# Optimization experiments

Hardware: AMD Instinct MI355X
Metric: run time of the kernel (lower is better)

Reference implementation:

```python
import jax, jax.numpy as jnp
import numpy as np

NH = 16  # num_attention_heads
DH = 64  # attention_head_size
HS = 1024
LN_EPS = 1e-5


def _linear(x, W, b):
    return jnp.einsum('bsh,oh->bso', x, W) + b


def _mha(q, k, v, mask):
    # q:[B,Sq,H] k,v:[B,Sk,H] mask:[B,Sk] int (1=keep,0=mask)
    B, Sq, _ = q.shape
    Sk = k.shape[1]
    qh = q.reshape(B, Sq, NH, DH).transpose(0, 2, 1, 3)
    kh = k.reshape(B, Sk, NH, DH).transpose(0, 2, 1, 3)
    vh = v.reshape(B, Sk, NH, DH).transpose(0, 2, 1, 3)
    scores = jnp.einsum('bhqd,bhkd->bhqk', qh, kh) / np.sqrt(DH).astype(np.float32)
    if mask is not None:
        scores = jnp.where(mask[:, None, None, :] == 0, jnp.float32(-1e9), scores)
    probs = jax.nn.softmax(scores, axis=-1)  # dropout is identity in eval
    ctx = jnp.einsum('bhqk,bhkd->bhqd', probs, vh)
    return ctx.transpose(0, 2, 1, 3).reshape(B, Sq, NH * DH)


def _layernorm(x, g, b):
    mu = jnp.mean(x, axis=-1, keepdims=True)
    var = jnp.mean(jnp.square(x - mu), axis=-1, keepdims=True)
    return (x - mu) * jax.lax.rsqrt(var + LN_EPS) * g + b


def setup_inputs() -> dict:
    key = jax.random.key(0)
    ks = jax.random.split(key, 20)
    B, Sc, Se = 4, 512, 2048
    s = 0.02
    inp = {
        'claim_embeddings': jax.random.normal(ks[0], (B, Sc, HS), jnp.float32),
        'evidence_embeddings': jax.random.normal(ks[1], (B, Se, HS), jnp.float32),
        'claim_mask': jax.random.randint(ks[2], (B, Sc), 0, 2, jnp.int32),
        'evidence_mask': jax.random.randint(ks[3], (B, Se), 0, 2, jnp.int32),
    }
    names = ['cq', 'ek', 'ev', 'eq', 'ck', 'cv']
    for i, n in enumerate(names):
        inp['W_' + n] = jax.random.normal(ks[4 + i], (HS, HS), jnp.float32) * s
        inp['b_' + n] = jnp.zeros((HS,), jnp.float32)
    inp['ln_g'] = jnp.ones((HS,), jnp.float32)
    inp['ln_b'] = jnp.zeros((HS,), jnp.float32)
    return inp


def reference(claim_embeddings, evidence_embeddings, claim_mask, evidence_mask,
              W_cq, b_cq, W_ek, b_ek, W_ev, b_ev,
              W_eq, b_eq, W_ck, b_ck, W_cv, b_cv, ln_g, ln_b):
    claim_att = _mha(_linear(claim_embeddings, W_cq, b_cq),
                     _linear(evidence_embeddings, W_ek, b_ek),
                     _linear(evidence_embeddings, W_ev, b_ev), evidence_mask)
    evid_att = _mha(_linear(evidence_embeddings, W_eq, b_eq),
                    _linear(claim_embeddings, W_ck, b_ck),
                    _linear(claim_embeddings, W_cv, b_cv), claim_mask)
    claim_out = _layernorm(claim_embeddings + claim_att, ln_g, ln_b)
    evid_out = _layernorm(evidence_embeddings + evid_att, ln_g, ln_b)
    return (claim_out, evid_out)
```

## Files before the change

kernel.cpp:

```cpp
#include <hip/hip_runtime.h>
#include <hip/hip_bf16.h>
#include <stdint.h>

typedef __hip_bfloat16 bf16;
typedef __attribute__((ext_vector_type(8))) short bf16x8;
typedef __attribute__((ext_vector_type(4))) float f32x4;

#define DEV __device__ __forceinline__

DEV float lo_bf(unsigned int v) { union { unsigned int u; float f; } c; c.u = v << 16; return c.f; }
DEV float hi_bf(unsigned int v) { union { unsigned int u; float f; } c; c.u = v & 0xffff0000u; return c.f; }
DEV float bs2f(short h) { union { unsigned int u; float f; } c; c.u = ((unsigned int)(unsigned short)h) << 16; return c.f; }

DEV int probe_bf16(const void* ln_g) { return ((const uint16_t*)ln_g)[0] == 0x3F80; }

DEV unsigned short f2bs(float f) { union { bf16 h; unsigned short s; } u; u.h = __float2bfloat16(f); return u.s; }

DEV float ldf(const void* p, size_t i, int bfm) {
    return bfm ? __bfloat162float(((const bf16*)p)[i]) : ((const float*)p)[i];
}

DEV bf16x8 pack8(float4 x, float4 y) {
    union { unsigned short s[8]; bf16x8 v; } u;
    u.s[0] = f2bs(x.x); u.s[1] = f2bs(x.y); u.s[2] = f2bs(x.z); u.s[3] = f2bs(x.w);
    u.s[4] = f2bs(y.x); u.s[5] = f2bs(y.y); u.s[6] = f2bs(y.z); u.s[7] = f2bs(y.w);
    return u.v;
}

DEV bf16x8 ld8cvt(const void* p, size_t i, int bfm) {
    if (bfm) return *(const bf16x8*)((const bf16*)p + i);
    const float4* f = (const float4*)((const float*)p + i);
    return pack8(f[0], f[1]);
}

DEV void gload_lds16(const bf16* g, bf16* l) {
    __builtin_amdgcn_global_load_lds(
        (const __attribute__((address_space(1))) void*)g,
        (__attribute__((address_space(3))) void*)l,
        16, 0, 0);
}

template<int CTRL>
DEV float dpp_ror(float x) {
    union { float f; int i; } u; u.f = x;
    const int r = __builtin_amdgcn_update_dpp(0, u.i, CTRL, 0xf, 0xf, false);
    union { int i; float f; } w; w.i = r; return w.f;
}

__global__ __launch_bounds__(256) void conv_bf16(
    const void* __restrict__ Xc, const void* __restrict__ Xe,
    const void* __restrict__ W0, const void* __restrict__ W1, const void* __restrict__ W2,
    const void* __restrict__ W3, const void* __restrict__ W4, const void* __restrict__ W5,
    bf16* __restrict__ dst, const void* __restrict__ probe)
{
    const int bfm = probe_bf16(probe);
    const size_t tot = (size_t)16384 * 1024;
    const size_t step = (size_t)gridDim.x * 256 * 8;
    for (size_t e = ((size_t)blockIdx.x * 256 + threadIdx.x) * 8; e < tot; e += step) {
        const size_t row = e >> 10;
        const void* src; size_t off;
        if (row < 2048)       { src = Xc; off = e; }
        else if (row < 10240) { src = Xe; off = e - (size_t)2048 * 1024; }
        else {
            const int wi = (int)((row - 10240) >> 10);
            src = (wi == 0) ? W0 : (wi == 1) ? W1 : (wi == 2) ? W2 :
                  (wi == 3) ? W3 : (wi == 4) ? W4 : W5;
            off = e - (size_t)(10240 + wi * 1024) * 1024;
        }
        *(bf16x8*)(dst + e) = ld8cvt(src, off, bfm);
    }
}

__global__ __launch_bounds__(256) void gemm_fast(
    const bf16* __restrict__ AW,
    const void* __restrict__ B0, const void* __restrict__ B1, const void* __restrict__ B2,
    const void* __restrict__ B3, const void* __restrict__ B4, const void* __restrict__ B5,
    bf16* __restrict__ Out, const void* __restrict__ probe)
{
    __shared__ __align__(16) bf16 As[2][128 * 32];
    __shared__ __align__(16) bf16 Bs[2][128 * 32];

    const int bfm = probe_bf16(probe);
    const int L = (blockIdx.x & 7) * 240 + (blockIdx.x >> 3);
    const int z  = L / 640;
    const int rem = L % 640;
    const int bx = rem >> 3;
    const int by = rem & 7;
    const int rowBase = bx * 128;
    const int colBase = by * 128;
    const int ev = rowBase >= 2048;
    const int widx = z * 2 + ev;

    const bf16* Ap = AW;
    const bf16* Wp = AW + (size_t)(10240 + widx * 1024) * 1024;
    const void* bias = (widx == 0) ? B0 : (widx == 1) ? B1 : (widx == 2) ? B2 :
                       (widx == 3) ? B3 : (widx == 4) ? B4 : B5;
    bf16* O = Out + (size_t)z * 10240 * 1024;

    const int tid  = threadIdx.x;
    const int wave = tid >> 6;
    const int lane = tid & 63;
    const int wm   = wave >> 1;
    const int wn   = wave & 1;
    const int quad = lane >> 4;
    const int l16  = lane & 15;

    f32x4 acc[4][4];
#pragma unroll
    for (int i = 0; i < 4; i++)
#pragma unroll
        for (int j = 0; j < 4; j++) acc[i][j] = (f32x4){0.f, 0.f, 0.f, 0.f};

    const int sr = tid >> 2;
    const int sc = (tid & 3) * 8;
    const size_t ga = (size_t)(rowBase + sr) * 1024 + sc;
    const size_t gb = (size_t)(colBase + sr) * 1024 + sc;

    auto stage = [&](int buf, int k0) {
        gload_lds16(Ap + ga + k0,                     &As[buf][tid * 8]);
        gload_lds16(Ap + ga + (size_t)64 * 1024 + k0, &As[buf][2048 + tid * 8]);
        gload_lds16(Wp + gb + k0,                     &Bs[buf][tid * 8]);
        gload_lds16(Wp + gb + (size_t)64 * 1024 + k0, &Bs[buf][2048 + tid * 8]);
    };

    stage(0, 0);
    __syncthreads();

    int cur = 0;
    for (int k0 = 0; k0 < 1024; k0 += 32) {
        if (k0 + 32 < 1024) stage(cur ^ 1, k0 + 32);

        bf16x8 af[4], bfr[4];
#pragma unroll
        for (int i = 0; i < 4; i++) {
            af[i]  = *(const bf16x8*)(&As[cur][(wm * 64 + i * 16 + l16) * 32 + quad * 8]);
            bfr[i] = *(const bf16x8*)(&Bs[cur][(wn * 64 + i * 16 + l16) * 32 + quad * 8]);
        }
#pragma unroll
        for (int i = 0; i < 4; i++)
#pragma unroll
            for (int j = 0; j < 4; j++)
                acc[i][j] = __builtin_amdgcn_mfma_f32_16x16x32_bf16(af[i], bfr[j], acc[i][j], 0, 0, 0);

        __syncthreads();
        cur ^= 1;
    }

#pragma unroll
    for (int j = 0; j < 4; j++) {
        const int col = colBase + wn * 64 + j * 16 + l16;
        const float bv = ldf(bias, col, bfm);
#pragma unroll
        for (int i = 0; i < 4; i++) {
            const int row0 = rowBase + wm * 64 + i * 16 + quad * 4;
#pragma unroll
            for (int rr = 0; rr < 4; rr++)
                O[(size_t)(row0 + rr) * 1024 + col] = __float2bfloat16(acc[i][j][rr] + bv);
        }
    }
}

DEV void attn_core(const bf16* __restrict__ Q, const bf16* __restrict__ K,
                   const bf16* __restrict__ V, const int* __restrict__ mask,
                   bf16* __restrict__ O, int Sk, int h, int qRow0)
{
    __shared__ __align__(16) short Ks [64 * 72];
    __shared__ __align__(16) short VTs[64 * 72];
    __shared__ __align__(16) short Ps [4][16 * 72];

    const int tid  = threadIdx.x;
    const int w    = tid >> 6;
    const int lane = tid & 63;
    const int quad = lane >> 4;
    const int l16  = lane & 15;
    const int qRow = qRow0 + w * 16 + l16;

    const short* Qp = (const short*)Q + (size_t)qRow * 1024 + h * 64;
    const bf16x8 qf0 = *(const bf16x8*)(Qp + quad * 8);
    const bf16x8 qf1 = *(const bf16x8*)(Qp + 32 + quad * 8);

    bf16x8 ones8;
#pragma unroll
    for (int i = 0; i < 8; i++) ones8[i] = (short)0x3F80;

    f32x4 oacc[4];
#pragma unroll
    for (int dt = 0; dt < 4; dt++) oacc[dt] = (f32x4){0.f, 0.f, 0.f, 0.f};
    f32x4 lacc = (f32x4){0.f, 0.f, 0.f, 0.f};
    float mrun[4] = {-3e38f, -3e38f, -3e38f, -3e38f};

    const int sn = tid >> 2, sseg = tid & 3;
    const int vn2 = (tid & 31) * 2;
    const int vdg = tid >> 5;

    bf16x8 pk0, pk1, pv0, pv1;
    auto loadkv = [&](int k0) {
        const short* src = (const short*)K + (size_t)(k0 + sn) * 1024 + h * 64 + sseg * 16;
        pk0 = *(const bf16x8*)src;
        pk1 = *(const bf16x8*)(src + 8);
        const short* vsrc = (const short*)V + (size_t)(k0 + vn2) * 1024 + h * 64 + vdg * 8;
        pv0 = *(const bf16x8*)vsrc;
        pv1 = *(const bf16x8*)(vsrc + 1024);
    };
    loadkv(0);

    const float SCL = 0.18033688f;

    for (int k0 = 0; k0 < Sk; k0 += 64) {
        __syncthreads();
        *(bf16x8*)(Ks + sn * 72 + sseg * 16)     = pk0;
        *(bf16x8*)(Ks + sn * 72 + sseg * 16 + 8) = pk1;
#pragma unroll
        for (int i = 0; i < 8; i++) {
            const unsigned int pr = (unsigned short)pv0[i] |
                                    ((unsigned int)(unsigned short)pv1[i] << 16);
            *(unsigned int*)(VTs + (vdg * 8 + i) * 72 + vn2) = pr;
        }
        __syncthreads();
        {
            int kn = k0 + 64; if (kn >= Sk) kn = 0;
            loadkv(kn);
        }

        const int mv_all = mask[k0 + lane];

        f32x4 sacc[4];
#pragma unroll
        for (int t = 0; t < 4; t++) {
            const bf16x8 kf0 = *(const bf16x8*)(Ks + (t * 16 + l16) * 72 + quad * 8);
            const bf16x8 kf1 = *(const bf16x8*)(Ks + (t * 16 + l16) * 72 + 32 + quad * 8);
            f32x4 s = (f32x4){0.f, 0.f, 0.f, 0.f};
            s = __builtin_amdgcn_mfma_f32_16x16x32_bf16(qf0, kf0, s, 0, 0, 0);
            s = __builtin_amdgcn_mfma_f32_16x16x32_bf16(qf1, kf1, s, 0, 0, 0);
            const int mv = __shfl(mv_all, t * 16 + l16);
#pragma unroll
            for (int r = 0; r < 4; r++) sacc[t][r] = mv ? s[r] * SCL : -1e9f;
        }

        float cmax[4];
#pragma unroll
        for (int r = 0; r < 4; r++) {
            cmax[r] = fmaxf(fmaxf(sacc[0][r], sacc[1][r]), fmaxf(sacc[2][r], sacc[3][r]));
            cmax[r] = fmaxf(cmax[r], dpp_ror<0x121>(cmax[r]));
            cmax[r] = fmaxf(cmax[r], dpp_ror<0x122>(cmax[r]));
            cmax[r] = fmaxf(cmax[r], dpp_ror<0x124>(cmax[r]));
            cmax[r] = fmaxf(cmax[r], dpp_ror<0x128>(cmax[r]));
        }

        float alpha[4];
#pragma unroll
        for (int r = 0; r < 4; r++) {
            const float mn = fmaxf(mrun[r], cmax[r]);
            alpha[r] = exp2f(mrun[r] - mn);
            mrun[r] = mn;
        }
#pragma unroll
        for (int t = 0; t < 4; t++)
#pragma unroll
            for (int r = 0; r < 4; r++) {
                const float p = exp2f(sacc[t][r] - mrun[r]);
                Ps[w][(quad * 4 + r) * 72 + t * 16 + l16] = f2bs(p);
            }
#pragma unroll
        for (int r = 0; r < 4; r++) lacc[r] *= alpha[r];
#pragma unroll
        for (int dt = 0; dt < 4; dt++)
#pragma unroll
            for (int r = 0; r < 4; r++) oacc[dt][r] *= alpha[r];


        const bf16x8 pa0 = *(const bf16x8*)(Ps[w] + l16 * 72 + quad * 8);
        const bf16x8 pa1 = *(const bf16x8*)(Ps[w] + l16 * 72 + 32 + quad * 8);
        lacc = __builtin_amdgcn_mfma_f32_16x16x32_bf16(pa0, ones8, lacc, 0, 0, 0);
        lacc = __builtin_amdgcn_mfma_f32_16x16x32_bf16(pa1, ones8, lacc, 0, 0, 0);
#pragma unroll
        for (int dt = 0; dt < 4; dt++) {
            const bf16x8 vb0 = *(const bf16x8*)(VTs + (dt * 16 + l16) * 72 + quad * 8);
            const bf16x8 vb1 = *(const bf16x8*)(VTs + (dt * 16 + l16) * 72 + 32 + quad * 8);
            oacc[dt] = __builtin_amdgcn_mfma_f32_16x16x32_bf16(pa0, vb0, oacc[dt], 0, 0, 0);
            oacc[dt] = __builtin_amdgcn_mfma_f32_16x16x32_bf16(pa1, vb1, oacc[dt], 0, 0, 0);
        }
    }

    short* Op = (short*)O;
#pragma unroll
    for (int r = 0; r < 4; r++) {
        const float inv = 1.0f / lacc[r];
        const size_t row = (size_t)(qRow0 + w * 16 + quad * 4 + r) * 1024 + h * 64;
#pragma unroll
        for (int dt = 0; dt < 4; dt++)
            Op[row + dt * 16 + l16] = f2bs(oacc[dt][r] * inv);
    }
}

__global__ __launch_bounds__(256) void attn_flat(
    const bf16* __restrict__ Q1, const bf16* __restrict__ K1, const bf16* __restrict__ V1,
    const int* __restrict__ m1, bf16* __restrict__ O1,
    const bf16* __restrict__ Q2, const bf16* __restrict__ K2, const bf16* __restrict__ V2,
    const int* __restrict__ m2, bf16* __restrict__ O2)
{
    const int xcd = blockIdx.x & 7;
    const int idx = blockIdx.x >> 3;
    const int grp = idx / 5;
    const int pos = idx % 5;

    if (pos == 0) {
        const int j = xcd * 64 + grp;
        const int b = j >> 7;
        const int h = (j >> 3) & 15;
        const int qRow0 = (j & 7) * 64;
        attn_core(Q1 + (size_t)b * 512 * 1024,
                  K1 + (size_t)b * 2048 * 1024,
                  V1 + (size_t)b * 2048 * 1024,
                  m1 + (size_t)b * 2048,
                  O1 + (size_t)b * 512 * 1024, 2048, h, qRow0);
    } else {
        const int j = xcd * 256 + grp * 4 + (pos - 1);
        const int b = j >> 9;
        const int h = (j >> 5) & 15;
        const int qRow0 = (j & 31) * 64;
        attn_core(Q2 + (size_t)b * 2048 * 1024,
                  K2 + (size_t)b * 512 * 1024,
                  V2 + (size_t)b * 512 * 1024,
                  m2 + (size_t)b * 512,
                  O2 + (size_t)b * 2048 * 1024, 512, h, qRow0);
    }
}

__global__ __launch_bounds__(256) void attn_dual(
    const bf16* __restrict__ Q1, const bf16* __restrict__ K1, const bf16* __restrict__ V1,
    const int* __restrict__ m1, bf16* __restrict__ O1,
    const bf16* __restrict__ Q2, const bf16* __restrict__ K2, const bf16* __restrict__ V2,
    const int* __restrict__ m2, bf16* __restrict__ O2)
{
    const int z = blockIdx.z;
    if (z < 4) {
        if (blockIdx.x >= 8) return;
        attn_core(Q1 + (size_t)z * 512 * 1024,
                  K1 + (size_t)z * 2048 * 1024,
                  V1 + (size_t)z * 2048 * 1024,
                  m1 + (size_t)z * 2048,
                  O1 + (size_t)z * 512 * 1024, 2048, blockIdx.y, blockIdx.x * 64);
    } else {
        const int b = z - 4;
        attn_core(Q2 + (size_t)b * 2048 * 1024,
                  K2 + (size_t)b * 512 * 1024,
                  V2 + (size_t)b * 512 * 1024,
                  m2 + (size_t)b * 512,
                  O2 + (size_t)b * 2048 * 1024, 512, blockIdx.y, blockIdx.x * 64);
    }
}

DEV void gemm_core(const void* __restrict__ A, int aRow0,
                   const void* __restrict__ W, const void* __restrict__ bias,
                   bf16* __restrict__ O, int bfm)
{
    __shared__ __align__(16) short As [128 * 40];
    __shared__ __align__(16) short Bsh[128 * 40];

    const int tid  = threadIdx.x;
    const int wave = tid >> 6;
    const int lane = tid & 63;
    const int wm   = wave >> 1;
    const int wn   = wave & 1;
    const int quad = lane >> 4;
    const int l16  = lane & 15;

    const int rowBase = blockIdx.x * 128;
    const int colBase = blockIdx.y * 128;

    f32x4 acc[4][4];
#pragma unroll
    for (int i = 0; i < 4; i++)
#pragma unroll
        for (int j = 0; j < 4; j++) acc[i][j] = (f32x4){0.f, 0.f, 0.f, 0.f};

    const int r  = tid >> 2;
    const int c8 = (tid & 3) * 8;
    const size_t aIdx = (size_t)(aRow0 + rowBase + r) * 1024 + c8;
    const size_t wIdx = (size_t)(colBase + r) * 1024 + c8;
    short* sA0 = As  + r * 40 + c8;
    short* sA1 = As  + (r + 64) * 40 + c8;
    short* sB0 = Bsh + r * 40 + c8;
    short* sB1 = Bsh + (r + 64) * 40 + c8;

    auto compute = [&]() {
        bf16x8 af[4], bfr[4];
#pragma unroll
        for (int i = 0; i < 4; i++) {
            af[i]  = *(const bf16x8*)(As  + (wm * 64 + i * 16 + l16) * 40 + quad * 8);
            bfr[i] = *(const bf16x8*)(Bsh + (wn * 64 + i * 16 + l16) * 40 + quad * 8);
        }
#pragma unroll
        for (int i = 0; i < 4; i++)
#pragma unroll
            for (int j = 0; j < 4; j++)
                acc[i][j] = __builtin_amdgcn_mfma_f32_16x16x32_bf16(af[i], bfr[j], acc[i][j], 0, 0, 0);
    };

    if (bfm) {
        const bf16* Ab = (const bf16*)A;
        const bf16* Wb = (const bf16*)W;
        bf16x8 ra0 = *(const bf16x8*)(Ab + aIdx);
        bf16x8 ra1 = *(const bf16x8*)(Ab + aIdx + (size_t)64 * 1024);
        bf16x8 rb0 = *(const bf16x8*)(Wb + wIdx);
        bf16x8 rb1 = *(const bf16x8*)(Wb + wIdx + (size_t)64 * 1024);
        for (int k0 = 0; k0 < 1024; k0 += 32) {
            __syncthreads();
            *(bf16x8*)sA0 = ra0; *(bf16x8*)sA1 = ra1;
            *(bf16x8*)sB0 = rb0; *(bf16x8*)sB1 = rb1;
            __syncthreads();
            const int kn = (k0 + 32) & 1023;
            ra0 = *(const bf16x8*)(Ab + aIdx + kn);
            ra1 = *(const bf16x8*)(Ab + aIdx + (size_t)64 * 1024 + kn);
            rb0 = *(const bf16x8*)(Wb + wIdx + kn);
            rb1 = *(const bf16x8*)(Wb + wIdx + (size_t)64 * 1024 + kn);
            compute();
        }
    } else {
        const float* Af = (const float*)A;
        const float* Wf = (const float*)W;
        float4 f[4][2];
        auto loadf = [&](int k) {
            f[0][0] = *(const float4*)(Af + aIdx + k);
            f[0][1] = *(const float4*)(Af + aIdx + k + 4);
            f[1][0] = *(const float4*)(Af + aIdx + (size_t)64 * 1024 + k);
            f[1][1] = *(const float4*)(Af + aIdx + (size_t)64 * 1024 + k + 4);
            f[2][0] = *(const float4*)(Wf + wIdx + k);
            f[2][1] = *(const float4*)(Wf + wIdx + k + 4);
            f[3][0] = *(const float4*)(Wf + wIdx + (size_t)64 * 1024 + k);
            f[3][1] = *(const float4*)(Wf + wIdx + (size_t)64 * 1024 + k + 4);
        };
        loadf(0);
        for (int k0 = 0; k0 < 1024; k0 += 32) {
            const bf16x8 ra0 = pack8(f[0][0], f[0][1]);
            const bf16x8 ra1 = pack8(f[1][0], f[1][1]);
            const bf16x8 rb0 = pack8(f[2][0], f[2][1]);
            const bf16x8 rb1 = pack8(f[3][0], f[3][1]);
            __syncthreads();
            *(bf16x8*)sA0 = ra0; *(bf16x8*)sA1 = ra1;
            *(bf16x8*)sB0 = rb0; *(bf16x8*)sB1 = rb1;
            __syncthreads();
            loadf((k0 + 32) & 1023);
            compute();
        }
    }

#pragma unroll
    for (int j = 0; j < 4; j++) {
        const int col = colBase + wn * 64 + j * 16 + l16;
        const float bv = ldf(bias, col, bfm);
#pragma unroll
        for (int i = 0; i < 4; i++) {
            const int row0 = rowBase + wm * 64 + i * 16 + quad * 4;
#pragma unroll
            for (int rr = 0; rr < 4; rr++)
                O[(size_t)(row0 + rr) * 1024 + col] = __float2bfloat16(acc[i][j][rr] + bv);
        }
    }
}

__global__ __launch_bounds__(256) void gemm_bt6(
    const void* __restrict__ Ac, const void* __restrict__ Ae,
    const void* __restrict__ W0, const void* __restrict__ W1, const void* __restrict__ W2,
    const void* __restrict__ W3, const void* __restrict__ W4, const void* __restrict__ W5,
    const void* __restrict__ B0, const void* __restrict__ B1, const void* __restrict__ B2,
    const void* __restrict__ B3, const void* __restrict__ B4, const void* __restrict__ B5,
    bf16* __restrict__ O0, bf16* __restrict__ O1, bf16* __restrict__ O2,
    bf16* __restrict__ O3, bf16* __restrict__ O4, bf16* __restrict__ O5,
    const void* __restrict__ dt_probe)
{
    const int z = blockIdx.z;
    if (z < 3 && blockIdx.x >= 16) return;
    const int bfm = probe_bf16(dt_probe);
    const void* A = (z < 3) ? Ac : Ae;
    const void* W    = (z == 0) ? W0 : (z == 1) ? W1 : (z == 2) ? W2 : (z == 3) ? W3 : (z == 4) ? W4 : W5;
    const void* bias = (z == 0) ? B0 : (z == 1) ? B1 : (z == 2) ? B2 : (z == 3) ? B3 : (z == 4) ? B4 : B5;
    bf16* O          = (z == 0) ? O0 : (z == 1) ? O1 : (z == 2) ? O2 : (z == 3) ? O3 : (z == 4) ? O4 : O5;
    gemm_core(A, 0, W, bias, O, bfm);
}

__global__ __launch_bounds__(256) void ln_wave(
    const void* __restrict__ Xc, const void* __restrict__ Xe, const bf16* __restrict__ Att,
    const void* __restrict__ G, const void* __restrict__ Bb, void* __restrict__ O)
{
    const int bfm = probe_bf16(G);
    const int lane = threadIdx.x & 63;
    const size_t row = (size_t)blockIdx.x * 4 + (threadIdx.x >> 6);
    const void* X; size_t xrow;
    if (row < 2048) { X = Xc; xrow = row; }
    else            { X = Xe; xrow = row - 2048; }

    const int e0 = lane * 16;
    float v[16];
    {
        const short* ap = (const short*)Att + row * 1024 + e0;
        const bf16x8 a0 = *(const bf16x8*)ap;
        const bf16x8 a1 = *(const bf16x8*)(ap + 8);
#pragma unroll
        for (int j = 0; j < 8; j++) { v[j] = bs2f(a0[j]); v[8 + j] = bs2f(a1[j]); }
    }
    if (bfm) {
        const short* xp = (const short*)X + xrow * 1024 + e0;
        const bf16x8 x0 = *(const bf16x8*)xp;
        const bf16x8 x1 = *(const bf16x8*)(xp + 8);
#pragma unroll
        for (int j = 0; j < 8; j++) { v[j] += bs2f(x0[j]); v[8 + j] += bs2f(x1[j]); }
    } else {
        const float* xp = (const float*)X + xrow * 1024 + e0;
#pragma unroll
        for (int q = 0; q < 4; q++) {
            const float4 f = *(const float4*)(xp + q * 4);
            v[q * 4 + 0] += f.x; v[q * 4 + 1] += f.y;
            v[q * 4 + 2] += f.z; v[q * 4 + 3] += f.w;
        }
    }

    float s = 0.f, ss = 0.f;
#pragma unroll
    for (int j = 0; j < 16; j++) { s += v[j]; ss += v[j] * v[j]; }
#pragma unroll
    for (int off = 32; off > 0; off >>= 1) {
        s  += __shfl_xor(s,  off);
        ss += __shfl_xor(ss, off);
    }
    const float mu   = s * (1.f / 1024.f);
    const float var  = ss * (1.f / 1024.f) - mu * mu;
    const float rstd = rsqrtf(var + 1e-5f);

    float g[16], bb[16];
    if (bfm) {
        const short* gp = (const short*)G + e0;
        const short* bp = (const short*)Bb + e0;
        const bf16x8 g0 = *(const bf16x8*)gp, g1 = *(const bf16x8*)(gp + 8);
        const bf16x8 b0 = *(const bf16x8*)bp, b1 = *(const bf16x8*)(bp + 8);
#pragma unroll
        for (int j = 0; j < 8; j++) {
            g[j] = bs2f(g0[j]); g[8 + j] = bs2f(g1[j]);
            bb[j] = bs2f(b0[j]); bb[8 + j] = bs2f(b1[j]);
        }
    } else {
        const float* gp = (const float*)G + e0;
        const float* bp = (const float*)Bb + e0;
#pragma unroll
        for (int q = 0; q < 4; q++) {
            const float4 gf = *(const float4*)(gp + q * 4);
            const float4 bf = *(const float4*)(bp + q * 4);
            g[q * 4 + 0] = gf.x; g[q * 4 + 1] = gf.y; g[q * 4 + 2] = gf.z; g[q * 4 + 3] = gf.w;
            bb[q * 4 + 0] = bf.x; bb[q * 4 + 1] = bf.y; bb[q * 4 + 2] = bf.z; bb[q * 4 + 3] = bf.w;
        }
    }

    float o[16];
#pragma unroll
    for (int j = 0; j < 16; j++) o[j] = (v[j] - mu) * rstd * g[j] + bb[j];

    const size_t obase = row * 1024 + e0;
    if (bfm) {
        union { unsigned short sh[16]; uint4 u[2]; } pk;
#pragma unroll
        for (int j = 0; j < 16; j++) pk.sh[j] = f2bs(o[j]);
        uint4* op = (uint4*)((bf16*)O + obase);
        op[0] = pk.u[0]; op[1] = pk.u[1];
    } else {
        float* op = (float*)O + obase;
#pragma unroll
        for (int q = 0; q < 4; q++)
            *(float4*)(op + q * 4) = (float4){o[q * 4], o[q * 4 + 1], o[q * 4 + 2], o[q * 4 + 3]};
    }
}

DEV void ln_body(const void* __restrict__ X, size_t xrow, const bf16* __restrict__ Att,
                 size_t arow, const void* __restrict__ G, const void* __restrict__ Bb,
                 void* __restrict__ O, size_t orow, int bfm)
{
    __shared__ float r1[4], r2[4];
    const int tid = threadIdx.x;
    const size_t abase = arow * 1024 + tid * 4;
    const size_t xbase = xrow * 1024 + tid * 4;
    const uint2 ab = *(const uint2*)(Att + abase);
    const float v0 = ldf(X, xbase + 0, bfm) + lo_bf(ab.x);
    const float v1 = ldf(X, xbase + 1, bfm) + hi_bf(ab.x);
    const float v2 = ldf(X, xbase + 2, bfm) + lo_bf(ab.y);
    const float v3 = ldf(X, xbase + 3, bfm) + hi_bf(ab.y);
    float s  = v0 + v1 + v2 + v3;
    float ss = v0 * v0 + v1 * v1 + v2 * v2 + v3 * v3;
    for (int off = 32; off > 0; off >>= 1) { s += __shfl_down(s, off); ss += __shfl_down(ss, off); }
    if ((tid & 63) == 0) { r1[tid >> 6] = s; r2[tid >> 6] = ss; }
    __syncthreads();
    const float S  = r1[0] + r1[1] + r1[2] + r1[3];
    const float SS = r2[0] + r2[1] + r2[2] + r2[3];
    const float mu   = S * (1.f / 1024.f);
    const float var  = SS * (1.f / 1024.f) - mu * mu;
    const float rstd = rsqrtf(var + 1e-5f);
    const float g0 = ldf(G, tid * 4 + 0, bfm), g1 = ldf(G, tid * 4 + 1, bfm);
    const float g2 = ldf(G, tid * 4 + 2, bfm), g3 = ldf(G, tid * 4 + 3, bfm);
    const float bb0 = ldf(Bb, tid * 4 + 0, bfm), bb1 = ldf(Bb, tid * 4 + 1, bfm);
    const float bb2 = ldf(Bb, tid * 4 + 2, bfm), bb3 = ldf(Bb, tid * 4 + 3, bfm);
    const float o0 = (v0 - mu) * rstd * g0 + bb0;
    const float o1 = (v1 - mu) * rstd * g1 + bb1;
    const float o2 = (v2 - mu) * rstd * g2 + bb2;
    const float o3 = (v3 - mu) * rstd * g3 + bb3;
    const size_t obase = orow * 1024 + tid * 4;
    if (bfm) {
        union { unsigned short s4[4]; uint2 u; } pack;
        pack.s4[0] = f2bs(o0); pack.s4[1] = f2bs(o1); pack.s4[2] = f2bs(o2); pack.s4[3] = f2bs(o3);
        *(uint2*)((bf16*)O + obase) = pack.u;
    } else {
        *(float4*)((float*)O + obase) = (float4){o0, o1, o2, o3};
    }
}

__global__ __launch_bounds__(256) void ln_kernel(
    const void* __restrict__ X, int xRow0, const bf16* __restrict__ Att,
    const void* __restrict__ G, const void* __restrict__ Bb,
    void* __restrict__ O, size_t oRow0)
{
    const int bfm = probe_bf16(G);
    const size_t row = blockIdx.x;
    ln_body(X, (size_t)xRow0 + row, Att, row, G, Bb, O, oRow0 + row, bfm);
}

extern "C" void kernel_launch(void* const* d_in, const int* in_sizes, int n_in,
                              void* d_out, int out_size, void* d_ws, size_t ws_size,
                              hipStream_t stream)
{
    (void)in_sizes; (void)n_in; (void)out_size;

    const void* c_emb  = d_in[0];
    const void* e_emb  = d_in[1];
    const int*  c_mask = (const int*)d_in[2];
    const int*  e_mask = (const int*)d_in[3];
    const void* W_cq = d_in[4];  const void* b_cq = d_in[5];
    const void* W_ek = d_in[6];  const void* b_ek = d_in[7];
    const void* W_ev = d_in[8];  const void* b_ev = d_in[9];
    const void* W_eq = d_in[10]; const void* b_eq = d_in[11];
    const void* W_ck = d_in[12]; const void* b_ck = d_in[13];
    const void* W_cv = d_in[14]; const void* b_cv = d_in[15];
    const void* ln_g = d_in[16]; const void* ln_b = d_in[17];

    const int B = 4, Scl = 512, Sev = 2048;
    const size_t MC = (size_t)B * Scl;
    const size_t ME = (size_t)B * Sev;
    const size_t MT = MC + ME;
    const size_t RW = MT * 1024;

    dim3 blk(256);
    const size_t need_fast = (3 * RW + (size_t)16384 * 1024) * sizeof(bf16);

    if (ws_size >= need_fast) {
        bf16* Qr = (bf16*)d_ws;
        bf16* Kr = Qr + RW;
        bf16* Vr = Kr + RW;
        bf16* CV = Vr + RW;

        conv_bf16<<<dim3(2048), blk, 0, stream>>>(
            c_emb, e_emb, W_cq, W_eq, W_ck, W_ek, W_cv, W_ev, CV, ln_g);

        gemm_fast<<<dim3(1920), blk, 0, stream>>>(
            CV, b_cq, b_eq, b_ck, b_ek, b_cv, b_ev, Qr, ln_g);

        attn_flat<<<dim3(2560), blk, 0, stream>>>(
            Qr,             Kr + MC * 1024, Vr + MC * 1024, e_mask, Qr,
            Qr + MC * 1024, Kr,             Vr,             c_mask, Qr + MC * 1024);

        ln_wave<<<dim3((unsigned)(MT / 4)), blk, 0, stream>>>(
            c_emb, e_emb, Qr, ln_g, ln_b, d_out);
    } else {
        bf16* q_c = (bf16*)d_ws;
        bf16* k_c = q_c + MC * 1024;
        bf16* v_c = k_c + MC * 1024;
        bf16* q_e = v_c + MC * 1024;
        bf16* k_e = q_e + ME * 1024;
        bf16* v_e = k_e + ME * 1024;

        gemm_bt6<<<dim3(64, 8, 6), blk, 0, stream>>>(
            c_emb, e_emb,
            W_cq, W_ck, W_cv, W_eq, W_ek, W_ev,
            b_cq, b_ck, b_cv, b_eq, b_ek, b_ev,
            q_c, k_c, v_c, q_e, k_e, v_e, ln_g);

        attn_dual<<<dim3(32, 16, 8), blk, 0, stream>>>(
            q_c, k_e, v_e, e_mask, q_c,
            q_e, k_c, v_c, c_mask, q_e);

        ln_kernel<<<dim3((unsigned)MC), blk, 0, stream>>>(
            c_emb, 0, q_c, ln_g, ln_b, d_out, 0);
        ln_kernel<<<dim3((unsigned)ME), blk, 0, stream>>>(
            e_emb, 0, q_e, ln_g, ln_b, d_out, MC);
    }
}
```

Baseline: 389.5 us.

## Stage GEMM and attention epilogues through LDS for coalesced stores; fold mask into MFMA init

The GEMM and attention epilogues now write their results into shared memory first and then emit 16-byte vectorized, coalesced global stores, instead of scattered 2-byte stores. The attention mask is applied as an additive bias in the MFMA accumulator initializer. The softmax scale is folded into an fmaf inside the native exp2 builtin, which removes a per-element select and multiply. These changes add extra __syncthreads and reuse of the staging LDS buffers. They also slightly change how masked scores interact with the scale (-1e9 is now scaled).

```diff
diff --git a/kernel.cpp b/kernel.cpp
--- a/kernel.cpp
+++ b/kernel.cpp
@@ -1,6 +1,7 @@
 #include <hip/hip_runtime.h>
 #include <hip/hip_bf16.h>
 #include <stdint.h>
+#include <math.h>
 
 typedef __hip_bfloat16 bf16;
 typedef __attribute__((ext_vector_type(8))) short bf16x8;
@@ -146,17 +147,30 @@
         cur ^= 1;
     }
 
+    bf16* Cme = (wn == 0) ? &As[0][0] : &Bs[0][0];
 #pragma unroll
     for (int j = 0; j < 4; j++) {
-        const int col = colBase + wn * 64 + j * 16 + l16;
-        const float bv = ldf(bias, col, bfm);
+        const int c64 = j * 16 + l16;
+        const float bv = ldf(bias, colBase + wn * 64 + c64, bfm);
 #pragma unroll
         for (int i = 0; i < 4; i++) {
-            const int row0 = rowBase + wm * 64 + i * 16 + quad * 4;
+            const int row0 = wm * 64 + i * 16 + quad * 4;
 #pragma unroll
             for (int rr = 0; rr < 4; rr++)
-                O[(size_t)(row0 + rr) * 1024 + col] = __float2bfloat16(acc[i][j][rr] + bv);
-        }
+                Cme[(row0 + rr) * 64 + c64] = __float2bfloat16(acc[i][j][rr] + bv);
+        }
+    }
+    __syncthreads();
+    const int srow = tid >> 3;
+    const int seg  = tid & 7;
+#pragma unroll
+    for (int pass = 0; pass < 4; pass++) {
+        const int row = pass * 32 + srow;
+        const bf16x8 v0 = *(const bf16x8*)(&As[0][0] + row * 64 + seg * 8);
+        const bf16x8 v1 = *(const bf16x8*)(&Bs[0][0] + row * 64 + seg * 8);
+        bf16* orow = O + (size_t)(rowBase + row) * 1024 + colBase;
+        *(bf16x8*)(orow + seg * 8)      = v0;
+        *(bf16x8*)(orow + 64 + seg * 8) = v1;
     }
 }
 
@@ -229,12 +243,11 @@
         for (int t = 0; t < 4; t++) {
             const bf16x8 kf0 = *(const bf16x8*)(Ks + (t * 16 + l16) * 72 + quad * 8);
             const bf16x8 kf1 = *(const bf16x8*)(Ks + (t * 16 + l16) * 72 + 32 + quad * 8);
-            f32x4 s = (f32x4){0.f, 0.f, 0.f, 0.f};
+            const float mb = __shfl(mv_all, t * 16 + l16) ? 0.f : -1e9f;
+            f32x4 s = (f32x4){mb, mb, mb, mb};
             s = __builtin_amdgcn_mfma_f32_16x16x32_bf16(qf0, kf0, s, 0, 0, 0);
             s = __builtin_amdgcn_mfma_f32_16x16x32_bf16(qf1, kf1, s, 0, 0, 0);
-            const int mv = __shfl(mv_all, t * 16 + l16);
-#pragma unroll
-            for (int r = 0; r < 4; r++) sacc[t][r] = mv ? s[r] * SCL : -1e9f;
+            sacc[t] = s;
         }
 
         float cmax[4];
@@ -247,18 +260,19 @@
             cmax[r] = fmaxf(cmax[r], dpp_ror<0x128>(cmax[r]));
         }
 
-        float alpha[4];
+        float alpha[4], mscl[4];
 #pragma unroll
         for (int r = 0; r < 4; r++) {
             const float mn = fmaxf(mrun[r], cmax[r]);
-            alpha[r] = exp2f(mrun[r] - mn);
+            alpha[r] = __builtin_amdgcn_exp2f((mrun[r] - mn) * SCL);
             mrun[r] = mn;
+            mscl[r] = mn * SCL;
         }
 #pragma unroll
         for (int t = 0; t < 4; t++)
 #pragma unroll
             for (int r = 0; r < 4; r++) {
-                const float p = exp2f(sacc[t][r] - mrun[r]);
+                const float p = __builtin_amdgcn_exp2f(fmaf(sacc[t][r], SCL, -mscl[r]));
                 Ps[w][(quad * 4 + r) * 72 + t * 16 + l16] = f2bs(p);
             }
 #pragma unroll
@@ -282,14 +296,24 @@
         }
     }
 
-    short* Op = (short*)O;
+    __syncthreads();
 #pragma unroll
     for (int r = 0; r < 4; r++) {
         const float inv = 1.0f / lacc[r];
-        const size_t row = (size_t)(qRow0 + w * 16 + quad * 4 + r) * 1024 + h * 64;
+        const int orow = w * 16 + quad * 4 + r;
 #pragma unroll
         for (int dt = 0; dt < 4; dt++)
-            Op[row + dt * 16 + l16] = f2bs(oacc[dt][r] * inv);
+            Ks[orow * 72 + dt * 16 + l16] = (short)f2bs(oacc[dt][r] * inv);
+    }
+    __syncthreads();
+    const int srow = tid >> 3;
+    const int seg  = tid & 7;
+    short* Op = (short*)O;
+#pragma unroll
+    for (int pass = 0; pass < 2; pass++) {
+        const int row = pass * 32 + srow;
+        const bf16x8 v = *(const bf16x8*)(Ks + row * 72 + seg * 8);
+        *(bf16x8*)(Op + (size_t)(qRow0 + row) * 1024 + h * 64 + seg * 8) = v;
     }
 }
 
```

Measured after the change: 379.2 us. 2.6% less time.
